# Optimization experiments

Measured on AMD Instinct MI355X. Metric: run time of the kernel, lower is better.

Reference implementation:

```python
import jax, jax.numpy as jnp
import numpy as np

B, L, C = 1, 1536, 768
H, DK, DV, F = 8, 64, 96, 96


def setup_inputs() -> dict:
    key = jax.random.key(0)
    ks = jax.random.split(key, 9)
    s = 0.02
    return {
        "x": jax.random.normal(ks[0], (B, L, C), jnp.float32),
        "Wq": jax.random.normal(ks[1], (C, H * DK), jnp.float32) * s,
        "Wk": jax.random.normal(ks[2], (C, H * DK), jnp.float32) * s,
        "Wv": jax.random.normal(ks[3], (C, H * DV), jnp.float32) * s,
        "Wout": jax.random.normal(ks[4], (H * DV, C), jnp.float32) * s,
        "bout": jnp.zeros((C,), jnp.float32),
        "Wpos": jax.random.normal(ks[5], (F, H * DK), jnp.float32) * s,
        "rel_content_bias": jax.random.normal(ks[6], (1, H, 1, DK), jnp.float32),
        "rel_pos_bias": jax.random.normal(ks[7], (1, H, 1, DK), jnp.float32),
    }


def central_mask_embed(n, features):
    # positions: -(n-1) .. n-1  -> (2n-1,)
    positions = jnp.arange(-(n - 1), n)
    # center widths: 2^1 - 1 .. 2^features - 1
    widths = jnp.float32(2.0) ** jnp.arange(1, features + 1, dtype=jnp.float32) - 1.0
    return (widths[None, :] > jnp.abs(positions).astype(jnp.float32)[:, None]).astype(jnp.float32)


def relative_shift(t):
    # t: (b, h, t1, t2) with t2 = 2*t1 - 1 -> (b, h, t1, t1)
    b, h, t1, t2 = t.shape
    t = jnp.pad(t, ((0, 0), (0, 0), (0, 0), (1, 0)))  # (b,h,t1,t2+1)
    t = t.reshape(b, h, t2 + 1, t1)[:, :, 1:, :]       # (b,h,t2,t1)
    t = t.reshape(b, h, t1, t2)
    return t[..., : (t2 + 2) // 2]


def reference(x, Wq, Wk, Wv, Wout, bout, Wpos, rel_content_bias, rel_pos_bias):
    b, n, _ = x.shape
    q = (x @ Wq).reshape(b, n, H, DK).transpose(0, 2, 1, 3)  # b h n d
    k = (x @ Wk).reshape(b, n, H, DK).transpose(0, 2, 1, 3)
    v = (x @ Wv).reshape(b, n, H, DV).transpose(0, 2, 1, 3)
    q = q / jnp.float32(DK) ** 0.5

    content_logits = jnp.einsum("bhid,bhjd->bhij", q + rel_content_bias, k)

    pos = central_mask_embed(n, F)                 # (2n-1, F)
    pos_k = (pos @ Wpos).reshape(2 * n - 1, H, DK).transpose(1, 0, 2)  # h (2n-1) d
    pos_logits = jnp.einsum("bhid,hjd->bhij", q + rel_pos_bias, pos_k)
    pos_logits = relative_shift(pos_logits)        # (b,h,n,n)

    attn = jax.nn.softmax(content_logits + pos_logits, axis=-1)
    out = jnp.einsum("bhij,bhjd->bhid", attn, v)   # b h n dv
    out = out.transpose(0, 2, 1, 3).reshape(b, n, H * DV)
    return out @ Wout + bout
```

## Files before the change

### kernel.cpp

```cpp
#include <hip/hip_runtime.h>
#include <stdint.h>

#define NTOK 1536
#define CDIM 768
#define NH 8
#define DKH 64
#define DVH 96
#define NF 96

typedef unsigned short u16;
typedef __attribute__((ext_vector_type(8))) short s16x8;
typedef __attribute__((ext_vector_type(4))) float f32x4;

__device__ __forceinline__ float b2f(u16 u) {
    union { uint32_t i; float f; } v; v.i = ((uint32_t)u) << 16; return v.f;
}
__device__ __forceinline__ u16 f2b(float f) {
    union { float f; uint32_t i; } v; v.f = f;
    uint32_t x = v.i;
    return (u16)((x + 0x7FFFu + ((x >> 16) & 1u)) >> 16);
}
__device__ __forceinline__ float ldin(const void* p, int i, int f32) {
    return f32 ? ((const float*)p)[i] : b2f(((const u16*)p)[i]);
}

__device__ __forceinline__ int probe_f32(const void* p) {
    const u16* a = (const u16*)p;
    int lane = threadIdx.x & 63;
    int bad = 0;
#pragma unroll
    for (int t = 0; t < 4; ++t) {
        float v = b2f(a[lane + t * 64]);
        if (!(fabsf(v) < 1e6f)) bad = 1;
    }
    return __ballot(bad) != 0ull;
}

#define FIDX(m, kk) ((((kk) >> 3) * 16 + (m)) * 8 + ((kk) & 7))

#define OFF_WSUF 16
#define OFF_S11  (OFF_WSUF + 5632)
#define OFF_QF   (OFF_S11 + 147456)
#define OFF_KF   (OFF_QF + 393216)
#define OFF_VF   (OFF_KF + 393216)
#define OFF_AOF  (OFF_VF + 589824)
#define OFF_XF   (OFF_AOF + 589824)
#define OFF_WF   (OFF_XF + 589824)
#define OFF_WOF  (OFF_WF + 688128)

__global__ __launch_bounds__(256) void prep(const void* __restrict__ x,
                                            const void* __restrict__ Wq,
                                            const void* __restrict__ Wk,
                                            const void* __restrict__ Wv,
                                            const void* __restrict__ Wout,
                                            const void* __restrict__ Wpos,
                                            float* __restrict__ ws) {
    int bx = blockIdx.x, tid = threadIdx.x;
    int wv = tid >> 6, L = tid & 63;

    if (bx < 144) {
        int f = probe_f32(x);
        u16* dst = (u16*)(ws + OFF_XF);
        int cbase = (bx * 4 + wv) * 4;
        int m = L & 15, kq = L >> 4;
        int srcs[4];
#pragma unroll
        for (int c = 0; c < 4; ++c) {
            int ch = cbase + c;
            int ti = ch / 24, kc = ch % 24;
            srcs[c] = (ti * 16 + m) * CDIM + kc * 32 + kq * 8;
        }
        if (f) {
            float4 a[4][2];
#pragma unroll
            for (int c = 0; c < 4; ++c) {
                const float* xp = (const float*)x + srcs[c];
                a[c][0] = *(const float4*)(xp);
                a[c][1] = *(const float4*)(xp + 4);
            }
#pragma unroll
            for (int c = 0; c < 4; ++c) {
                union { u16 u[8]; uint4 v; } pk;
                pk.u[0] = f2b(a[c][0].x); pk.u[1] = f2b(a[c][0].y);
                pk.u[2] = f2b(a[c][0].z); pk.u[3] = f2b(a[c][0].w);
                pk.u[4] = f2b(a[c][1].x); pk.u[5] = f2b(a[c][1].y);
                pk.u[6] = f2b(a[c][1].z); pk.u[7] = f2b(a[c][1].w);
                *(uint4*)(dst + (cbase + c) * 512 + L * 8) = pk.v;
            }
        } else {
            uint4 v[4];
#pragma unroll
            for (int c = 0; c < 4; ++c) v[c] = *(const uint4*)((const u16*)x + srcs[c]);
#pragma unroll
            for (int c = 0; c < 4; ++c)
                *(uint4*)(dst + (cbase + c) * 512 + L * 8) = v[c];
        }
        return;
    }
    if (bx < 1104) {
        int c = (bx - 144) * 4 + wv;
        const void* src; int ld, cn0; u16* dst; int kc;
        if (c < 2688) {
            int tn = c / 24; kc = c % 24;
            int n0 = tn * 16;
            dst = (u16*)(ws + OFF_WF) + c * 512;
            if (n0 < 512)       { src = Wq; ld = 512;  cn0 = n0; }
            else if (n0 < 1024) { src = Wk; ld = 512;  cn0 = n0 - 512; }
            else                { src = Wv; ld = CDIM; cn0 = n0 - 1024; }
        } else {
            int c2 = c - 2688;
            int tn = c2 / 24; kc = c2 % 24;
            dst = (u16*)(ws + OFF_WOF) + c2 * 512;
            src = Wout; ld = CDIM; cn0 = tn * 16;
        }
        int f = probe_f32(src);
        int nn = L & 15, kq = L >> 4;
        int base = (kc * 32 + kq * 8) * ld + cn0 + nn;
        union { u16 u[8]; uint4 v; } pk;
        if (f) {
            const float* sp = (const float*)src + base;
            float a0 = sp[0], a1 = sp[ld], a2 = sp[2 * ld], a3 = sp[3 * ld];
            float a4 = sp[4 * ld], a5 = sp[5 * ld], a6 = sp[6 * ld], a7 = sp[7 * ld];
            pk.u[0] = f2b(a0); pk.u[1] = f2b(a1); pk.u[2] = f2b(a2); pk.u[3] = f2b(a3);
            pk.u[4] = f2b(a4); pk.u[5] = f2b(a5); pk.u[6] = f2b(a6); pk.u[7] = f2b(a7);
        } else {
            const u16* sp = (const u16*)src + base;
            pk.u[0] = sp[0]; pk.u[1] = sp[ld]; pk.u[2] = sp[2 * ld]; pk.u[3] = sp[3 * ld];
            pk.u[4] = sp[4 * ld]; pk.u[5] = sp[5 * ld]; pk.u[6] = sp[6 * ld]; pk.u[7] = sp[7 * ld];
        }
        *(uint4*)(dst + L * 8) = pk.v;
        return;
    }
    int t = bx - 1104;
    int f = probe_f32(Wpos);
    for (int hd = tid; hd < 512; hd += 256) {
        float s0 = 0.f, s1 = 0.f, s2 = 0.f, s3 = 0.f;
        int f0 = t;
        for (; f0 + 4 <= NF; f0 += 4) {
            s0 += ldin(Wpos, f0 * 512 + hd, f);
            s1 += ldin(Wpos, (f0 + 1) * 512 + hd, f);
            s2 += ldin(Wpos, (f0 + 2) * 512 + hd, f);
            s3 += ldin(Wpos, (f0 + 3) * 512 + hd, f);
        }
        for (; f0 < NF; ++f0) s0 += ldin(Wpos, f0 * 512 + hd, f);
        ws[OFF_WSUF + t * 512 + hd] = (s0 + s1) + (s2 + s3);
    }
}

__global__ __launch_bounds__(256) void qkv_reg(const void* __restrict__ rcb,
                                               const void* __restrict__ rpb,
                                               float* __restrict__ ws) {
    __shared__ float qt[64 * 68];
    __shared__ float rpd[12];
    const u16* xf = (const u16*)(ws + OFF_XF);
    const u16* wf = (const u16*)(ws + OFF_WF);
    u16* qf = (u16*)(ws + OFF_QF);
    u16* kf = (u16*)(ws + OFF_KF);
    u16* vf = (u16*)(ws + OFF_VF);

    int tid = threadIdx.x;
    int lane = tid & 63, w = tid >> 6;
    int quad = lane >> 4, col = lane & 15;
    int ti4 = blockIdx.x;
    int tn4 = blockIdx.y;
    int tn = tn4 * 4 + w;
    int i0 = ti4 * 64;
    bool isQ = (tn4 < 8);
    int hq = tn4;

    s16x8 bw0, bw1;
    int f32p = 0, f32c = 0;
    if (isQ) {
        f32p = probe_f32(rpb);
        f32c = probe_f32(rcb);
        int t = lane & 15, kq = lane >> 4;
        union { u16 u[8]; s16x8 v; } p0, p1;
#pragma unroll
        for (int j = 0; j < 8; ++j) {
            float v0 = 0.f, v1 = 0.f;
            if (t < 11) {
                v0 = ws[OFF_WSUF + t * 512 + hq * 64 + kq * 8 + j];
                v1 = ws[OFF_WSUF + t * 512 + hq * 64 + 32 + kq * 8 + j];
            }
            p0.u[j] = f2b(v0); p1.u[j] = f2b(v1);
        }
        bw0 = p0.v; bw1 = p1.v;
        if (tid < 12) {
            float s = 0.f;
            if (tid < 11) {
                const float* wp = ws + OFF_WSUF + tid * 512 + hq * 64;
                for (int d = 0; d < 64; ++d) s += ldin(rpb, hq * 64 + d, f32p) * wp[d];
            }
            rpd[tid] = s;
        }
    }

    f32x4 acc[4];
#pragma unroll
    for (int mt = 0; mt < 4; ++mt) acc[mt] = (f32x4){0.f, 0.f, 0.f, 0.f};

    const u16* bp = wf + (tn * 24) * 512 + lane * 8;
    const u16* ap = xf + (ti4 * 4 * 24) * 512 + lane * 8;
#pragma unroll 4
    for (int kc = 0; kc < 24; ++kc) {
        s16x8 bfrag = *(const s16x8*)(bp + kc * 512);
#pragma unroll
        for (int mt = 0; mt < 4; ++mt) {
            s16x8 afrag = *(const s16x8*)(ap + (mt * 24 + kc) * 512);
            acc[mt] = __builtin_amdgcn_mfma_f32_16x16x32_bf16(afrag, bfrag, acc[mt], 0, 0, 0);
        }
    }

    if (isQ) {
#pragma unroll
        for (int mt = 0; mt < 4; ++mt)
#pragma unroll
            for (int r = 0; r < 4; ++r)
                qt[(mt * 16 + quad * 4 + r) * 68 + w * 16 + col] = acc[mt][r] * 0.125f;
        __syncthreads();
        int m = lane & 15, kq = lane >> 4;
#pragma unroll
        for (int kc2 = 0; kc2 < 2; ++kc2) {
            union { u16 u[8]; uint4 v; } pk;
#pragma unroll
            for (int j = 0; j < 8; ++j) {
                int d = kc2 * 32 + kq * 8 + j;
                pk.u[j] = f2b(qt[(w * 16 + m) * 68 + d] + ldin(rcb, hq * 64 + d, f32c));
            }
            *(uint4*)(qf + (((hq * 96 + ti4 * 4 + w) * 2 + kc2) * 512) + lane * 8) = pk.v;
        }
        union { u16 u[8]; s16x8 v; } qa0, qa1;
#pragma unroll
        for (int j = 0; j < 8; ++j) {
            qa0.u[j] = f2b(qt[(w * 16 + m) * 68 + kq * 8 + j]);
            qa1.u[j] = f2b(qt[(w * 16 + m) * 68 + 32 + kq * 8 + j]);
        }
        f32x4 s11a = (f32x4){0.f, 0.f, 0.f, 0.f};
        s11a = __builtin_amdgcn_mfma_f32_16x16x32_bf16(qa0.v, bw0, s11a, 0, 0, 0);
        s11a = __builtin_amdgcn_mfma_f32_16x16x32_bf16(qa1.v, bw1, s11a, 0, 0, 0);
        if (col < 12) {
            float rp = rpd[col];
            float* s11 = ws + OFF_S11;
#pragma unroll
            for (int r = 0; r < 4; ++r)
                s11[(hq * NTOK + i0 + w * 16 + quad * 4 + r) * 12 + col] = s11a[r] + rp;
        }
    } else if (tn < 64) {
        int h = (tn >> 2) - 8;
        int d = ((tn & 3) * 16) + col;
#pragma unroll
        for (int mt = 0; mt < 4; ++mt) {
            int tj = ti4 * 4 + mt;
#pragma unroll
            for (int r = 0; r < 4; ++r) {
                int nn = quad * 4 + r;
                kf[((h * 96 + tj) * 2 + (d >> 5)) * 512 + FIDX(nn, d & 31)] = f2b(acc[mt][r]);
            }
        }
    } else {
        int c = tn * 16 + col - 1024;
        int h = c / 96, d = c % 96;
        int nt = d >> 4, nn = d & 15;
#pragma unroll
        for (int mt = 0; mt < 4; ++mt) {
#pragma unroll
            for (int r = 0; r < 4; ++r) {
                int j = i0 + mt * 16 + quad * 4 + r;
                int jc = j >> 5, kk = j & 31;
                vf[((h * 48 + jc) * 6 + nt) * 512 + FIDX(nn, kk)] = f2b(acc[mt][r]);
            }
        }
    }
}

__global__ __launch_bounds__(512) void attn_mfma(float* __restrict__ ws) {
    __shared__ float s11b[192];
    __shared__ float lw[8][16];
    __shared__ union {
        alignas(16) u16 pbuf[8][16 * 36];
        float Om[8][16 * 96];
    } sh;

    const u16* qf = (const u16*)(ws + OFF_QF);
    const u16* kf = (const u16*)(ws + OFF_KF);
    const u16* vf = (const u16*)(ws + OFF_VF);
    const float* s11 = ws + OFF_S11;
    u16* aof = (u16*)(ws + OFF_AOF);

    int h = blockIdx.x & 7;
    int ti = blockIdx.x >> 3;
    int i0 = ti * 16;
    int tid = threadIdx.x;
    int wv = tid >> 6, lane = tid & 63;
    int quad = lane >> 4, col = lane & 15;

    if (tid < 192) s11b[tid] = s11[(h * NTOK + i0 + tid / 12) * 12 + tid % 12];
    const u16* qp = qf + ((h * 96 + ti) * 2) * 512 + lane * 8;
    s16x8 a_lo = *(const s16x8*)(qp);
    s16x8 a_hi = *(const s16x8*)(qp + 512);
    __syncthreads();

    f32x4 O[6];
    float lsum[4];
#pragma unroll
    for (int nt = 0; nt < 6; ++nt) O[nt] = (f32x4){0.f, 0.f, 0.f, 0.f};
#pragma unroll
    for (int r = 0; r < 4; ++r) lsum[r] = 0.f;

    const u16* kbase = kf + ((h * 96 + wv * 12) * 2) * 512 + lane * 8;
    s16x8 k0lo = *(const s16x8*)(kbase);
    s16x8 k0hi = *(const s16x8*)(kbase + 512);
    s16x8 k1lo = *(const s16x8*)(kbase + 1024);
    s16x8 k1hi = *(const s16x8*)(kbase + 1536);

    for (int c = 0; c < 6; ++c) {
        f32x4 t0 = (f32x4){0.f, 0.f, 0.f, 0.f};
        f32x4 t1 = (f32x4){0.f, 0.f, 0.f, 0.f};
        t0 = __builtin_amdgcn_mfma_f32_16x16x32_bf16(a_lo, k0lo, t0, 0, 0, 0);
        t0 = __builtin_amdgcn_mfma_f32_16x16x32_bf16(a_hi, k0hi, t0, 0, 0, 0);
        t1 = __builtin_amdgcn_mfma_f32_16x16x32_bf16(a_lo, k1lo, t1, 0, 0, 0);
        t1 = __builtin_amdgcn_mfma_f32_16x16x32_bf16(a_hi, k1hi, t1, 0, 0, 0);
        if (c < 5) {
            const u16* kn = kbase + (c + 1) * 2048;
            k0lo = *(const s16x8*)(kn);
            k0hi = *(const s16x8*)(kn + 512);
            k1lo = *(const s16x8*)(kn + 1024);
            k1hi = *(const s16x8*)(kn + 1536);
        }
        int j0 = wv * 192 + c * 32;
        int lo1 = j0 - (i0 + 15), lo2 = i0 - (j0 + 31);
        int dmin = lo1 > 0 ? lo1 : (lo2 > 0 ? lo2 : 0);
        int dm1 = i0 + 15 - j0, dm2 = j0 + 31 - i0;
        int dmax = dm1 > dm2 ? dm1 : dm2;
        int tlo = 31 - __builtin_clz(dmin + 1);
        int thi = 31 - __builtin_clz(dmax + 1);
        if (tlo == thi) {
#pragma unroll
            for (int r = 0; r < 4; ++r) {
                int row = quad * 4 + r;
                float bv = s11b[row * 12 + tlo] - 12.f;
                float p0 = __expf(t0[r] + bv);
                float p1 = __expf(t1[r] + bv);
                sh.pbuf[wv][row * 36 + col] = f2b(p0);
                sh.pbuf[wv][row * 36 + 16 + col] = f2b(p1);
                lsum[r] += p0 + p1;
            }
        } else {
#pragma unroll
            for (int r = 0; r < 4; ++r) {
                int row = quad * 4 + r;
                int ig = i0 + row;
                int d0 = ig - (j0 + col); d0 = d0 < 0 ? -d0 : d0;
                int d1 = ig - (j0 + 16 + col); d1 = d1 < 0 ? -d1 : d1;
                float v0 = t0[r] + s11b[row * 12 + (31 - __builtin_clz(d0 + 1))];
                float v1 = t1[r] + s11b[row * 12 + (31 - __builtin_clz(d1 + 1))];
                float p0 = __expf(v0 - 12.f);
                float p1 = __expf(v1 - 12.f);
                sh.pbuf[wv][row * 36 + col] = f2b(p0);
                sh.pbuf[wv][row * 36 + 16 + col] = f2b(p1);
                lsum[r] += p0 + p1;
            }
        }
        int jc = wv * 6 + c;
        const u16* pr = &sh.pbuf[wv][col * 36 + quad * 8];
        union { s16x8 v; uint2 u2[2]; } pa;
        pa.u2[0] = *(const uint2*)(pr);
        pa.u2[1] = *(const uint2*)(pr + 4);
        const u16* vp = vf + ((h * 48 + jc) * 6) * 512 + lane * 8;
#pragma unroll
        for (int nt = 0; nt < 6; ++nt) {
            s16x8 vfr = *(const s16x8*)(vp + nt * 512);
            O[nt] = __builtin_amdgcn_mfma_f32_16x16x32_bf16(pa.v, vfr, O[nt], 0, 0, 0);
        }
    }

#pragma unroll
    for (int off = 1; off < 16; off <<= 1)
#pragma unroll
        for (int r = 0; r < 4; ++r) lsum[r] += __shfl_xor(lsum[r], off);
    if (col == 0)
#pragma unroll
        for (int r = 0; r < 4; ++r) lw[wv][quad * 4 + r] = lsum[r];
    __syncthreads();
#pragma unroll
    for (int r = 0; r < 4; ++r) {
        int row = quad * 4 + r;
#pragma unroll
        for (int nt = 0; nt < 6; ++nt)
            sh.Om[wv][row * 96 + nt * 16 + col] = O[nt][r];
    }
    __syncthreads();
    for (int idx = tid; idx < 16 * 96; idx += 512) {
        int row = idx / 96, cc = idx % 96;
        float L = 0.f, val = 0.f;
#pragma unroll
        for (int v = 0; v < 8; ++v) { L += lw[v][row]; val += sh.Om[v][idx]; }
        aof[(ti * 24 + h * 3 + (cc >> 5)) * 512 + FIDX(row, cc & 31)] = f2b(val / L);
    }
}

__global__ __launch_bounds__(256) void out_reg(const void* __restrict__ bout,
                                               float* __restrict__ ws,
                                               float* __restrict__ out) {
    const u16* af = (const u16*)(ws + OFF_AOF);
    const u16* wof = (const u16*)(ws + OFF_WOF);
    int f32b = probe_f32(bout);

    int tid = threadIdx.x;
    int lane = tid & 63, w = tid >> 6;
    int quad = lane >> 4, col = lane & 15;
    int ti4 = blockIdx.x;
    int tn = blockIdx.y * 4 + w;
    int i0 = ti4 * 64;
    int n0 = blockIdx.y * 64;

    f32x4 acc[4];
#pragma unroll
    for (int mt = 0; mt < 4; ++mt) acc[mt] = (f32x4){0.f, 0.f, 0.f, 0.f};

    const u16* bp = wof + (tn * 24) * 512 + lane * 8;
    const u16* ap = af + (ti4 * 4 * 24) * 512 + lane * 8;
#pragma unroll 4
    for (int kc = 0; kc < 24; ++kc) {
        s16x8 bfrag = *(const s16x8*)(bp + kc * 512);
#pragma unroll
        for (int mt = 0; mt < 4; ++mt) {
            s16x8 afrag = *(const s16x8*)(ap + (mt * 24 + kc) * 512);
            acc[mt] = __builtin_amdgcn_mfma_f32_16x16x32_bf16(afrag, bfrag, acc[mt], 0, 0, 0);
        }
    }

    int c = n0 + w * 16 + col;
    float bias = ldin(bout, c, f32b);
#pragma unroll
    for (int mt = 0; mt < 4; ++mt) {
#pragma unroll
        for (int r = 0; r < 4; ++r) {
            int i = i0 + mt * 16 + quad * 4 + r;
            out[i * CDIM + c] = acc[mt][r] + bias;
        }
    }
}

extern "C" void kernel_launch(void* const* d_in, const int* in_sizes, int n_in,
                              void* d_out, int out_size, void* d_ws, size_t ws_size,
                              hipStream_t stream) {
    float* out = (float*)d_out;
    float* ws = (float*)d_ws;

    const int want[9] = {1179648, 393216, 393216, 589824, 589824, 768, 49152, 512, 512};
    int role2in[9], used[9] = {0};
    bool ok = (n_in == 9);
    if (ok) {
        for (int r = 0; r < 9; ++r) {
            int found = -1;
            for (int i = 0; i < 9 && found < 0; ++i)
                if (!used[i] && in_sizes[i] == want[r]) found = i;
            if (found < 0) { ok = false; break; }
            used[found] = 1;
            role2in[r] = found;
        }
    }
    if (!ok) for (int r = 0; r < 9; ++r) role2in[r] = r;

    const void* x    = d_in[role2in[0]];
    const void* Wq   = d_in[role2in[1]];
    const void* Wk   = d_in[role2in[2]];
    const void* Wv   = d_in[role2in[3]];
    const void* Wout = d_in[role2in[4]];
    const void* bout = d_in[role2in[5]];
    const void* Wpos = d_in[role2in[6]];
    const void* rcb  = d_in[role2in[7]];
    const void* rpb  = d_in[role2in[8]];

    hipLaunchKernelGGL(prep, dim3(1115), dim3(256), 0, stream,
                       x, Wq, Wk, Wv, Wout, Wpos, ws);
    hipLaunchKernelGGL(qkv_reg, dim3(24, 28), dim3(256), 0, stream,
                       rcb, rpb, ws);
    hipLaunchKernelGGL(attn_mfma, dim3(768), dim3(512), 0, stream, ws);
    hipLaunchKernelGGL(out_reg, dim3(24, 12), dim3(256), 0, stream,
                       bout, ws, out);
}
```

Before: 147.6 us.

## Fuse four launches into two cooperative kernels with grid barriers

Merges prep with the QKV projection, and attention with the output projection, into two persistent cooperative kernels. Each pair is separated by a software grid barrier built from atomic counters at the start of the workspace, which is zeroed by a memset on every call. This is meant to remove two kernel launch boundaries and their tail gaps. In exchange it adds barrier spin cost, a memset, and a dependence on enough co-resident blocks for a cooperative launch, with the original four launches kept as a fallback.

Measured after the change: 147.2 us. No clear change (-0.3%).

```diff
diff --git a/kernel.cpp b/kernel.cpp
--- a/kernel.cpp
+++ b/kernel.cpp
@@ -38,7 +38,7 @@
 
 #define FIDX(m, kk) ((((kk) >> 3) * 16 + (m)) * 8 + ((kk) & 7))
 
-#define OFF_WSUF 16
+#define OFF_WSUF 1024
 #define OFF_S11  (OFF_WSUF + 5632)
 #define OFF_QF   (OFF_S11 + 147456)
 #define OFF_KF   (OFF_QF + 393216)
@@ -47,6 +47,30 @@
 #define OFF_XF   (OFF_AOF + 589824)
 #define OFF_WF   (OFF_XF + 589824)
 #define OFF_WOF  (OFF_WF + 688128)
+
+__device__ __forceinline__ void gbar_arrive(int* cbase, int bid) {
+    __threadfence();
+    __syncthreads();
+    if (threadIdx.x == 0)
+        __hip_atomic_fetch_add(&cbase[(bid & 7) * 32], 1,
+                               __ATOMIC_RELEASE, __HIP_MEMORY_SCOPE_AGENT);
+}
+__device__ __forceinline__ void gbar_wait(int* cbase, int expected) {
+    if (threadIdx.x == 0) {
+        long spins = 0;
+        int total;
+        do {
+            total = 0;
+#pragma unroll
+            for (int s = 0; s < 8; ++s)
+                total += __hip_atomic_load(&cbase[s * 32],
+                                           __ATOMIC_ACQUIRE, __HIP_MEMORY_SCOPE_AGENT);
+            if (total < expected) __builtin_amdgcn_s_sleep(32);
+        } while (total < expected && ++spins < (1L << 22));
+    }
+    __syncthreads();
+    __threadfence();
+}
 
 __global__ __launch_bounds__(256) void prep(const void* __restrict__ x,
                                             const void* __restrict__ Wq,
@@ -147,11 +171,102 @@
     }
 }
 
-__global__ __launch_bounds__(256) void qkv_reg(const void* __restrict__ rcb,
-                                               const void* __restrict__ rpb,
-                                               float* __restrict__ ws) {
-    __shared__ float qt[64 * 68];
-    __shared__ float rpd[12];
+__device__ __forceinline__ void prep_unit(int u, const void* x, const void* Wq,
+                                          const void* Wk, const void* Wv,
+                                          const void* Wout, const void* Wpos,
+                                          float* ws) {
+    int tid = threadIdx.x;
+    int wv = tid >> 6, L = tid & 63;
+    if (u < 144) {
+        int f = probe_f32(x);
+        u16* dst = (u16*)(ws + OFF_XF);
+        int cbase = (u * 4 + wv) * 4;
+        int m = L & 15, kq = L >> 4;
+        int srcs[4];
+#pragma unroll
+        for (int c = 0; c < 4; ++c) {
+            int ch = cbase + c;
+            int ti = ch / 24, kc = ch % 24;
+            srcs[c] = (ti * 16 + m) * CDIM + kc * 32 + kq * 8;
+        }
+        if (f) {
+            float4 a[4][2];
+#pragma unroll
+            for (int c = 0; c < 4; ++c) {
+                const float* xp = (const float*)x + srcs[c];
+                a[c][0] = *(const float4*)(xp);
+                a[c][1] = *(const float4*)(xp + 4);
+            }
+#pragma unroll
+            for (int c = 0; c < 4; ++c) {
+                union { u16 uu[8]; uint4 v; } pk;
+                pk.uu[0] = f2b(a[c][0].x); pk.uu[1] = f2b(a[c][0].y);
+                pk.uu[2] = f2b(a[c][0].z); pk.uu[3] = f2b(a[c][0].w);
+                pk.uu[4] = f2b(a[c][1].x); pk.uu[5] = f2b(a[c][1].y);
+                pk.uu[6] = f2b(a[c][1].z); pk.uu[7] = f2b(a[c][1].w);
+                *(uint4*)(dst + (cbase + c) * 512 + L * 8) = pk.v;
+            }
+        } else {
+            uint4 v[4];
+#pragma unroll
+            for (int c = 0; c < 4; ++c) v[c] = *(const uint4*)((const u16*)x + srcs[c]);
+#pragma unroll
+            for (int c = 0; c < 4; ++c)
+                *(uint4*)(dst + (cbase + c) * 512 + L * 8) = v[c];
+        }
+    } else if (u < 1104) {
+        int c = (u - 144) * 4 + wv;
+        const void* src; int ld, cn0; u16* dst; int kc;
+        if (c < 2688) {
+            int tn = c / 24; kc = c % 24;
+            int n0 = tn * 16;
+            dst = (u16*)(ws + OFF_WF) + c * 512;
+            if (n0 < 512)       { src = Wq; ld = 512;  cn0 = n0; }
+            else if (n0 < 1024) { src = Wk; ld = 512;  cn0 = n0 - 512; }
+            else                { src = Wv; ld = CDIM; cn0 = n0 - 1024; }
+        } else {
+            int c2 = c - 2688;
+            int tn = c2 / 24; kc = c2 % 24;
+            dst = (u16*)(ws + OFF_WOF) + c2 * 512;
+            src = Wout; ld = CDIM; cn0 = tn * 16;
+        }
+        int f = probe_f32(src);
+        int nn = L & 15, kq = L >> 4;
+        int base = (kc * 32 + kq * 8) * ld + cn0 + nn;
+        union { u16 uu[8]; uint4 v; } pk;
+        if (f) {
+            const float* sp = (const float*)src + base;
+            float a0 = sp[0], a1 = sp[ld], a2 = sp[2 * ld], a3 = sp[3 * ld];
+            float a4 = sp[4 * ld], a5 = sp[5 * ld], a6 = sp[6 * ld], a7 = sp[7 * ld];
+            pk.uu[0] = f2b(a0); pk.uu[1] = f2b(a1); pk.uu[2] = f2b(a2); pk.uu[3] = f2b(a3);
+            pk.uu[4] = f2b(a4); pk.uu[5] = f2b(a5); pk.uu[6] = f2b(a6); pk.uu[7] = f2b(a7);
+        } else {
+            const u16* sp = (const u16*)src + base;
+            pk.uu[0] = sp[0]; pk.uu[1] = sp[ld]; pk.uu[2] = sp[2 * ld]; pk.uu[3] = sp[3 * ld];
+            pk.uu[4] = sp[4 * ld]; pk.uu[5] = sp[5 * ld]; pk.uu[6] = sp[6 * ld]; pk.uu[7] = sp[7 * ld];
+        }
+        *(uint4*)(dst + L * 8) = pk.v;
+    } else {
+        int t = u - 1104;
+        int f = probe_f32(Wpos);
+        for (int hd = tid; hd < 512; hd += 256) {
+            float s0 = 0.f, s1 = 0.f, s2 = 0.f, s3 = 0.f;
+            int f0 = t;
+            for (; f0 + 4 <= NF; f0 += 4) {
+                s0 += ldin(Wpos, f0 * 512 + hd, f);
+                s1 += ldin(Wpos, (f0 + 1) * 512 + hd, f);
+                s2 += ldin(Wpos, (f0 + 2) * 512 + hd, f);
+                s3 += ldin(Wpos, (f0 + 3) * 512 + hd, f);
+            }
+            for (; f0 < NF; ++f0) s0 += ldin(Wpos, f0 * 512 + hd, f);
+            ws[OFF_WSUF + t * 512 + hd] = (s0 + s1) + (s2 + s3);
+        }
+    }
+}
+
+__device__ __forceinline__ void qkv_body(int ti4, int tn4,
+                                         const void* rcb, const void* rpb,
+                                         float* ws, float* qt, float* rpd) {
     const u16* xf = (const u16*)(ws + OFF_XF);
     const u16* wf = (const u16*)(ws + OFF_WF);
     u16* qf = (u16*)(ws + OFF_QF);
@@ -161,8 +276,6 @@
     int tid = threadIdx.x;
     int lane = tid & 63, w = tid >> 6;
     int quad = lane >> 4, col = lane & 15;
-    int ti4 = blockIdx.x;
-    int tn4 = blockIdx.y;
     int tn = tn4 * 4 + w;
     int i0 = ti4 * 64;
     bool isQ = (tn4 < 8);
@@ -273,28 +386,36 @@
     }
 }
 
-__global__ __launch_bounds__(512) void attn_mfma(float* __restrict__ ws) {
-    __shared__ float s11b[192];
-    __shared__ float lw[8][16];
-    __shared__ union {
+__global__ __launch_bounds__(256) void qkv_reg(const void* __restrict__ rcb,
+                                               const void* __restrict__ rpb,
+                                               float* __restrict__ ws) {
+    __shared__ float qt[64 * 68];
+    __shared__ float rpd[12];
+    qkv_body(blockIdx.x, blockIdx.y, rcb, rpb, ws, qt, rpd);
+}
+
+struct AttnSh {
+    float s11b[192];
+    float lw[8][16];
+    union {
         alignas(16) u16 pbuf[8][16 * 36];
         float Om[8][16 * 96];
-    } sh;
-
+    };
+};
+
+__device__ __forceinline__ void attn_body(int h, int ti, float* ws, AttnSh* sh) {
     const u16* qf = (const u16*)(ws + OFF_QF);
     const u16* kf = (const u16*)(ws + OFF_KF);
     const u16* vf = (const u16*)(ws + OFF_VF);
     const float* s11 = ws + OFF_S11;
     u16* aof = (u16*)(ws + OFF_AOF);
 
-    int h = blockIdx.x & 7;
-    int ti = blockIdx.x >> 3;
     int i0 = ti * 16;
     int tid = threadIdx.x;
     int wv = tid >> 6, lane = tid & 63;
     int quad = lane >> 4, col = lane & 15;
 
-    if (tid < 192) s11b[tid] = s11[(h * NTOK + i0 + tid / 12) * 12 + tid % 12];
+    if (tid < 192) sh->s11b[tid] = s11[(h * NTOK + i0 + tid / 12) * 12 + tid % 12];
     const u16* qp = qf + ((h * 96 + ti) * 2) * 512 + lane * 8;
     s16x8 a_lo = *(const s16x8*)(qp);
     s16x8 a_hi = *(const s16x8*)(qp + 512);
@@ -338,11 +459,11 @@
 #pragma unroll
             for (int r = 0; r < 4; ++r) {
                 int row = quad * 4 + r;
-                float bv = s11b[row * 12 + tlo] - 12.f;
+                float bv = sh->s11b[row * 12 + tlo] - 12.f;
                 float p0 = __expf(t0[r] + bv);
                 float p1 = __expf(t1[r] + bv);
-                sh.pbuf[wv][row * 36 + col] = f2b(p0);
-                sh.pbuf[wv][row * 36 + 16 + col] = f2b(p1);
+                sh->pbuf[wv][row * 36 + col] = f2b(p0);
+                sh->pbuf[wv][row * 36 + 16 + col] = f2b(p1);
                 lsum[r] += p0 + p1;
             }
         } else {
@@ -352,17 +473,17 @@
                 int ig = i0 + row;
                 int d0 = ig - (j0 + col); d0 = d0 < 0 ? -d0 : d0;
                 int d1 = ig - (j0 + 16 + col); d1 = d1 < 0 ? -d1 : d1;
-                float v0 = t0[r] + s11b[row * 12 + (31 - __builtin_clz(d0 + 1))];
-                float v1 = t1[r] + s11b[row * 12 + (31 - __builtin_clz(d1 + 1))];
+                float v0 = t0[r] + sh->s11b[row * 12 + (31 - __builtin_clz(d0 + 1))];
+                float v1 = t1[r] + sh->s11b[row * 12 + (31 - __builtin_clz(d1 + 1))];
                 float p0 = __expf(v0 - 12.f);
                 float p1 = __expf(v1 - 12.f);
-                sh.pbuf[wv][row * 36 + col] = f2b(p0);
-                sh.pbuf[wv][row * 36 + 16 + col] = f2b(p1);
+                sh->pbuf[wv][row * 36 + col] = f2b(p0);
+                sh->pbuf[wv][row * 36 + 16 + col] = f2b(p1);
                 lsum[r] += p0 + p1;
             }
         }
         int jc = wv * 6 + c;
-        const u16* pr = &sh.pbuf[wv][col * 36 + quad * 8];
+        const u16* pr = &sh->pbuf[wv][col * 36 + quad * 8];
         union { s16x8 v; uint2 u2[2]; } pa;
         pa.u2[0] = *(const uint2*)(pr);
         pa.u2[1] = *(const uint2*)(pr + 4);
@@ -380,39 +501,40 @@
         for (int r = 0; r < 4; ++r) lsum[r] += __shfl_xor(lsum[r], off);
     if (col == 0)
 #pragma unroll
-        for (int r = 0; r < 4; ++r) lw[wv][quad * 4 + r] = lsum[r];
+        for (int r = 0; r < 4; ++r) sh->lw[wv][quad * 4 + r] = lsum[r];
     __syncthreads();
 #pragma unroll
     for (int r = 0; r < 4; ++r) {
         int row = quad * 4 + r;
 #pragma unroll
         for (int nt = 0; nt < 6; ++nt)
-            sh.Om[wv][row * 96 + nt * 16 + col] = O[nt][r];
+            sh->Om[wv][row * 96 + nt * 16 + col] = O[nt][r];
     }
     __syncthreads();
     for (int idx = tid; idx < 16 * 96; idx += 512) {
         int row = idx / 96, cc = idx % 96;
         float L = 0.f, val = 0.f;
 #pragma unroll
-        for (int v = 0; v < 8; ++v) { L += lw[v][row]; val += sh.Om[v][idx]; }
+        for (int v = 0; v < 8; ++v) { L += sh->lw[v][row]; val += sh->Om[v][idx]; }
         aof[(ti * 24 + h * 3 + (cc >> 5)) * 512 + FIDX(row, cc & 31)] = f2b(val / L);
     }
 }
 
-__global__ __launch_bounds__(256) void out_reg(const void* __restrict__ bout,
-                                               float* __restrict__ ws,
-                                               float* __restrict__ out) {
+__global__ __launch_bounds__(512) void attn_mfma(float* __restrict__ ws) {
+    __shared__ AttnSh sh;
+    attn_body(blockIdx.x & 7, blockIdx.x >> 3, ws, &sh);
+}
+
+__device__ __forceinline__ void out_body256(int ti4, int by, int t2, int f32b,
+                                            const void* bout, float* ws,
+                                            float* out) {
     const u16* af = (const u16*)(ws + OFF_AOF);
     const u16* wof = (const u16*)(ws + OFF_WOF);
-    int f32b = probe_f32(bout);
-
-    int tid = threadIdx.x;
-    int lane = tid & 63, w = tid >> 6;
+    int lane = t2 & 63, w = t2 >> 6;
     int quad = lane >> 4, col = lane & 15;
-    int ti4 = blockIdx.x;
-    int tn = blockIdx.y * 4 + w;
+    int tn = by * 4 + w;
     int i0 = ti4 * 64;
-    int n0 = blockIdx.y * 64;
+    int n0 = by * 64;
 
     f32x4 acc[4];
 #pragma unroll
@@ -440,6 +562,62 @@
             out[i * CDIM + c] = acc[mt][r] + bias;
         }
     }
+}
+
+__global__ __launch_bounds__(256) void out_reg(const void* __restrict__ bout,
+                                               float* __restrict__ ws,
+                                               float* __restrict__ out) {
+    int f32b = probe_f32(bout);
+    out_body256(blockIdx.x, blockIdx.y, threadIdx.x, f32b, bout, ws, out);
+}
+
+__global__ __launch_bounds__(256) void fused_pq2(const void* __restrict__ x,
+                                                 const void* __restrict__ Wq,
+                                                 const void* __restrict__ Wk,
+                                                 const void* __restrict__ Wv,
+                                                 const void* __restrict__ Wout,
+                                                 const void* __restrict__ Wpos,
+                                                 const void* __restrict__ rcb,
+                                                 const void* __restrict__ rpb,
+                                                 float* __restrict__ ws) {
+    __shared__ float qt[64 * 68];
+    __shared__ float rpd[12];
+    int bid = blockIdx.x;
+
+    for (int u = bid; u < 1115; u += gridDim.x)
+        prep_unit(u, x, Wq, Wk, Wv, Wout, Wpos, ws);
+
+    int* c1 = (int*)ws;
+    gbar_arrive(c1, bid);
+    if (bid >= 672) return;
+    gbar_wait(c1, (int)gridDim.x);
+
+    for (int u = bid; u < 672; u += gridDim.x) {
+        qkv_body(u % 24, u / 24, rcb, rpb, ws, qt, rpd);
+        __syncthreads();
+    }
+}
+
+__global__ __launch_bounds__(512) void fused_ao2(const void* __restrict__ bout,
+                                                 float* __restrict__ ws,
+                                                 float* __restrict__ out) {
+    __shared__ AttnSh sh;
+    int bid = blockIdx.x, tid = threadIdx.x;
+
+    for (int u = bid; u < 768; u += gridDim.x) {
+        attn_body(u & 7, u >> 3, ws, &sh);
+        __syncthreads();
+    }
+
+    int* c2 = (int*)ws + 256;
+    gbar_arrive(c2, bid);
+    if (bid >= 144) return;
+    gbar_wait(c2, (int)gridDim.x);
+
+    int f32b = probe_f32(bout);
+    int half = tid >> 8, t2 = tid & 255;
+    for (int u = bid * 2 + half; u < 288; u += gridDim.x * 2)
+        out_body256(u % 24, u / 24, t2, f32b, bout, ws, out);
 }
 
 extern "C" void kernel_launch(void* const* d_in, const int* in_sizes, int n_in,
@@ -473,11 +651,52 @@
     const void* rcb  = d_in[role2in[7]];
     const void* rpb  = d_in[role2in[8]];
 
-    hipLaunchKernelGGL(prep, dim3(1115), dim3(256), 0, stream,
-                       x, Wq, Wk, Wv, Wout, Wpos, ws);
-    hipLaunchKernelGGL(qkv_reg, dim3(24, 28), dim3(256), 0, stream,
-                       rcb, rpb, ws);
-    hipLaunchKernelGGL(attn_mfma, dim3(768), dim3(512), 0, stream, ws);
-    hipLaunchKernelGGL(out_reg, dim3(24, 12), dim3(256), 0, stream,
-                       bout, ws, out);
-}
+    static int inited = 0;
+    static int G1 = 0, G2 = 0;
+    if (!inited) {
+        int nCU = 256, occ1 = 0, occ2 = 0;
+        hipDeviceProp_t prop;
+        int dev = 0;
+        (void)hipGetDevice(&dev);
+        if (hipGetDeviceProperties(&prop, dev) == hipSuccess && prop.multiProcessorCount > 0)
+            nCU = prop.multiProcessorCount;
+        if (hipOccupancyMaxActiveBlocksPerMultiprocessor(&occ1, fused_pq2, 256, 0) == hipSuccess
+            && occ1 > 0) {
+            G1 = occ1 * nCU; if (G1 > 1115) G1 = 1115;
+            if (G1 < 672) G1 = 0;
+        }
+        if (hipOccupancyMaxActiveBlocksPerMultiprocessor(&occ2, fused_ao2, 512, 0) == hipSuccess
+            && occ2 > 0) {
+            G2 = occ2 * nCU; if (G2 > 768) G2 = 768;
+            if (G2 < 288) G2 = 0;
+        }
+        inited = 1;
+    }
+
+    if (G1 > 0 || G2 > 0)
+        hipMemsetAsync(d_ws, 0, 4096, stream);
+
+    bool doneA = false, doneB = false;
+    if (G1 > 0) {
+        void* argsA[] = {(void*)&x, (void*)&Wq, (void*)&Wk, (void*)&Wv, (void*)&Wout,
+                         (void*)&Wpos, (void*)&rcb, (void*)&rpb, (void*)&ws};
+        doneA = hipLaunchCooperativeKernel(fused_pq2, dim3(G1), dim3(256),
+                                           argsA, 0, stream) == hipSuccess;
+    }
+    if (!doneA) {
+        hipLaunchKernelGGL(prep, dim3(1115), dim3(256), 0, stream,
+                           x, Wq, Wk, Wv, Wout, Wpos, ws);
+        hipLaunchKernelGGL(qkv_reg, dim3(24, 28), dim3(256), 0, stream,
+                           rcb, rpb, ws);
+    }
+    if (G2 > 0) {
+        void* argsB[] = {(void*)&bout, (void*)&ws, (void*)&out};
+        doneB = hipLaunchCooperativeKernel(fused_ao2, dim3(G2), dim3(512),
+                                           argsB, 0, stream) == hipSuccess;
+    }
+    if (!doneB) {
+        hipLaunchKernelGGL(attn_mfma, dim3(768), dim3(512), 0, stream, ws);
+        hipLaunchKernelGGL(out_reg, dim3(24, 12), dim3(256), 0, stream,
+                           bout, ws, out);
+    }
+}
```
